# Kernel optimization log

Measured on AMD Instinct MI355X. Metric: run time of the kernel, lower is better.

## Reference

```python
import jax, jax.numpy as jnp
import numpy as np
from jax import lax

QBITS = 8  # per layer_configs: 8-bit weights and activations


def fake_quant(x, bits=QBITS):
    """Per-tensor symmetric fake quantization with straight-through estimator."""
    qmax = float(2 ** (bits - 1) - 1)  # 127 for 8-bit
    scale = jnp.maximum(jnp.max(jnp.abs(x)), 1e-8) / qmax
    q = jnp.clip(jnp.round(x / scale), -qmax - 1.0, qmax) * scale
    # STE: forward uses q, backward passes gradient through unchanged
    return x + lax.stop_gradient(q - x)


def qconv(x, w, b):
    """Fake-quantized conv: quantize activations and weights, then VALID conv + bias."""
    xq = fake_quant(x)
    wq = fake_quant(w)
    y = lax.conv_general_dilated(
        xq, wq, window_strides=(1, 1), padding='VALID',
        dimension_numbers=('NCHW', 'OIHW', 'NCHW'))
    return y + b[None, :, None, None]


def setup_inputs() -> dict:
    key = jax.random.key(0)
    ks = jax.random.split(key, 9)
    return {
        'x':  jax.random.uniform(ks[0], (256, 1, 128, 128), dtype=jnp.float32),
        'w1': jax.random.normal(ks[1], (16, 1, 3, 3), dtype=jnp.float32) * 0.3,
        'b1': jax.random.normal(ks[2], (16,), dtype=jnp.float32) * 0.05,
        'w2': jax.random.normal(ks[3], (16, 16, 3, 3), dtype=jnp.float32) * 0.1,
        'b2': jax.random.normal(ks[4], (16,), dtype=jnp.float32) * 0.05,
        'w3': jax.random.normal(ks[5], (16, 16, 3, 3), dtype=jnp.float32) * 0.1,
        'b3': jax.random.normal(ks[6], (16,), dtype=jnp.float32) * 0.05,
        'w4': jax.random.normal(ks[7], (1, 16, 2, 2), dtype=jnp.float32) * 0.1,
        'b4': jax.random.normal(ks[8], (1,), dtype=jnp.float32) * 0.05,
    }


def reference(x, w1, b1, w2, b2, w3, b3, w4, b4):
    # x: [N,1,128,128] -> [N,16,126,126] -> [N,16,124,124] -> [N,16,122,122] -> [N,1,121,121]
    h = jax.nn.relu(qconv(x, w1, b1))
    h = jax.nn.relu(qconv(h, w2, b2))
    h = jax.nn.relu(qconv(h, w3, b3))
    return jax.nn.sigmoid(qconv(h, w4, b4))
```

## Files before the change

### kernel.cpp

```cpp
#include <hip/hip_runtime.h>
#include <math.h>


#define THREADS 256

typedef __attribute__((ext_vector_type(4))) int i32x4;

__device__ __forceinline__ int xcd_swz(int bid, int nwg) {
    return (bid & 7) * (nwg >> 3) + (bid >> 3);
}

__device__ __forceinline__ float block_reduce_max(float m, float* wred) {
#pragma unroll
    for (int off = 32; off > 0; off >>= 1)
        m = fmaxf(m, __shfl_down(m, off, 64));
    if ((threadIdx.x & 63) == 0) wred[threadIdx.x >> 6] = m;
    __syncthreads();
    return fmaxf(fmaxf(wred[0], wred[1]), fmaxf(wred[2], wred[3]));
}

__global__ void init_kernel(unsigned int* slots) {
    if (threadIdx.x < 8) slots[threadIdx.x] = 0u;
}

__global__ void fill_kernel(float* out, int n, float v) {
    int i = blockIdx.x * blockDim.x + threadIdx.x;
    int stride = gridDim.x * blockDim.x;
    for (; i < n; i += stride) out[i] = v;
}

__global__ __launch_bounds__(THREADS) void absmax4_kernel(
    const float4* __restrict__ x, int n4, unsigned int* __restrict__ slot) {
    __shared__ float wred[4];
    float m = 0.f;
    const int stride = gridDim.x * blockDim.x;
    for (int i = blockIdx.x * blockDim.x + threadIdx.x; i < n4; i += stride) {
        float4 v = x[i];
        m = fmaxf(fmaxf(fabsf(v.x), fabsf(v.y)),
                  fmaxf(fmaxf(fabsf(v.z), fabsf(v.w)), m));
    }
    m = block_reduce_max(m, wred);
    if (threadIdx.x == 0) atomicMax(slot, __float_as_uint(m));
}

__global__ __launch_bounds__(THREADS) void quant_w_kernel(
    const float* __restrict__ w1, const float* __restrict__ w2,
    const float* __restrict__ w3, const float* __restrict__ w4,
    float* __restrict__ qw1, float* __restrict__ qw4,
    signed char* __restrict__ wi8_2, signed char* __restrict__ wi8_3,
    unsigned int* __restrict__ slots) {
    __shared__ float wred[4];
    const float* w; int nel;
    switch (blockIdx.x) {
        case 0:  w = w1; nel = 144;  break;
        case 1:  w = w2; nel = 2304; break;
        case 2:  w = w3; nel = 2304; break;
        default: w = w4; nel = 64;   break;
    }
    float m = 0.f;
    for (int i = threadIdx.x; i < nel; i += blockDim.x)
        m = fmaxf(m, fabsf(w[i]));
    m = block_reduce_max(m, wred);
    if (threadIdx.x == 0) slots[4 + blockIdx.x] = __float_as_uint(m);
    const float s = fmaxf(m, 1e-8f) / 127.0f;

    if (blockIdx.x == 0) {
        for (int i = threadIdx.x; i < 144; i += blockDim.x) {
            int p = i % 9, o = i / 9;
            float q = fminf(fmaxf(rintf(w[i] / s), -128.f), 127.f);
            qw1[p * 16 + o] = q * s;
        }
    } else if (blockIdx.x == 3) {
        for (int i = threadIdx.x; i < 64; i += blockDim.x) {
            float q = fminf(fmaxf(rintf(w[i] / s), -128.f), 127.f);
            qw4[i] = q * s;
        }
    } else {
        signed char* wi8 = (blockIdx.x == 1) ? wi8_2 : wi8_3;
        for (int i = threadIdx.x; i < 3072; i += blockDim.x) {
            int ci = i & 15, lane = (i >> 4) & 63, g = i >> 10;
            int co = lane & 15, qq = lane >> 4;
            int pos = 4 * g + qq;
            float v = 0.f;
            if (pos < 9) {
                int ky = pos / 3, kx = pos % 3;
                v = fminf(fmaxf(rintf(w[((co * 16 + ci) * 3 + ky) * 3 + kx] / s),
                                -128.f), 127.f);
            }
            wi8[i] = (signed char)(int)v;
        }
    }
}

template <int MODE>
__global__ __launch_bounds__(THREADS) void conv1_kernel(
    const float* __restrict__ x, const float* __restrict__ qw,
    const float* __restrict__ bias, signed char* __restrict__ out,
    unsigned int* __restrict__ slots) {
    constexpr int IH = 128, IW = 128, OH = 126, OW = 126;
    __shared__ float tile[34 * 34];
    __shared__ float wred[4];
    const int bid = xcd_swz(blockIdx.x, gridDim.x);
    const int n = bid >> 4, tr = bid & 15;
    const int oy0 = (tr >> 2) * 32, ox0 = (tr & 3) * 32;
    const float s_in = fmaxf(__uint_as_float(slots[0]), 1e-8f) / 127.0f;
    const float* xN = x + (size_t)n * IH * IW;

#pragma unroll
    for (int it = 0; it < 5; ++it) {
        int px = it * 256 + threadIdx.x;
        if (px < 1156) {
            int iy = px / 34, ix = px - iy * 34;
            int gy = min(oy0 + iy, IH - 1), gx = min(ox0 + ix, IW - 1);
            float q = rintf(xN[gy * IW + gx] / s_in);
            tile[px] = fminf(fmaxf(q, -128.f), 127.f);
        }
    }
    __syncthreads();

    const int tx = (threadIdx.x & 15) * 2, ty = (threadIdx.x >> 4) * 2;
    float m = 0.f;
    float s_out = 0.f;
    if constexpr (MODE == 2)
        s_out = fmaxf(__uint_as_float(slots[1]), 1e-8f) / 127.0f;

#pragma unroll
    for (int sy = 0; sy < 2; ++sy)
#pragma unroll
    for (int sx = 0; sx < 2; ++sx) {
        const int py = ty + sy, pxx = tx + sx;
        float acc[16];
#pragma unroll
        for (int c = 0; c < 16; ++c) acc[c] = 0.f;
#pragma unroll
        for (int p = 0; p < 9; ++p) {
            const float xv = tile[(py + p / 3) * 34 + pxx + p % 3];
            const float* wp = qw + p * 16;
#pragma unroll
            for (int co = 0; co < 16; ++co)
                acc[co] = fmaf(xv, wp[co], acc[co]);
        }
        const int oy = oy0 + py, ox = ox0 + pxx;
        const bool ok = (oy < OH) && (ox < OW);
        if constexpr (MODE == 1) {
#pragma unroll
            for (int co = 0; co < 16; ++co) {
                float y = fmaxf(fmaf(acc[co], s_in, bias[co]), 0.f);
                if (ok) m = fmaxf(m, y);
            }
        } else {
            unsigned pk[4] = {0u, 0u, 0u, 0u};
#pragma unroll
            for (int co = 0; co < 16; ++co) {
                float y = fmaxf(fmaf(acc[co], s_in, bias[co]), 0.f);
                float q8 = fminf(fmaxf(rintf(y / s_out), -128.f), 127.f);
                pk[co >> 2] |= ((unsigned)(int)q8 & 0xffu) << ((co & 3) * 8);
            }
            if (ok) {
                int4 v; v.x = pk[0]; v.y = pk[1]; v.z = pk[2]; v.w = pk[3];
                *(int4*)(out + ((size_t)(n * OH + oy) * OW + ox) * 16) = v;
            }
        }
    }
    if constexpr (MODE == 1) {
        m = block_reduce_max(m, wred);
        if (threadIdx.x == 0) atomicMax(&slots[1], __float_as_uint(m));
    }
}

template <bool STORE>
__global__ __launch_bounds__(THREADS) void mconv_kernel(
    const signed char* __restrict__ in, const signed char* __restrict__ wi8,
    const float* __restrict__ bias, signed char* __restrict__ out,
    unsigned int* __restrict__ slots, int in_slot, int w_slot, int out_slot,
    int IH, int IW) {
    __shared__ signed char tile[1156 * 16];
    __shared__ float wred[4];
    const int OH = IH - 2, OW = IW - 2;
    const int bid = xcd_swz(blockIdx.x, gridDim.x);
    const int n = bid >> 4, tr = bid & 15;
    const int oy0 = (tr >> 2) * 32, ox0 = (tr & 3) * 32;

    const int tid = threadIdx.x, lane = tid & 63, wv = tid >> 6;
    const int q = lane >> 4, col = lane & 15;

    const signed char* inN = in + (size_t)n * IH * IW * 16;

#pragma unroll
    for (int it = 0; it < 5; ++it) {
        int px = it * 256 + tid;
        if (px < 1156) {
            int iy = px / 34, ix = px - iy * 34;
            int gy = min(oy0 + iy, IH - 1), gx = min(ox0 + ix, IW - 1);
            *(int4*)(tile + px * 16) =
                *(const int4*)(inN + ((size_t)gy * IW + gx) * 16);
        }
    }

    i32x4 afrag[3];
#pragma unroll
    for (int g = 0; g < 3; ++g)
        afrag[g] = ((const i32x4*)wi8)[g * 64 + lane];

    __syncthreads();

    int poff[3];
#pragma unroll
    for (int g = 0; g < 3; ++g) {
        int pos = 4 * g + q;
        int dy = (pos < 9) ? pos / 3 : 0;
        int dx = (pos < 9) ? pos % 3 : 0;
        poff[g] = (dy * 34 + dx) * 16;
    }
    const int wr = wv >> 1, wc = wv & 1;
    const int bx = 16 * wc + col;
    const int ox = ox0 + bx;

    const float s_in = fmaxf(__uint_as_float(slots[in_slot]), 1e-8f) / 127.0f;
    const float s_w  = fmaxf(__uint_as_float(slots[w_slot]),  1e-8f) / 127.0f;
    const float sxw = s_in * s_w;
    float bj[4];
#pragma unroll
    for (int j = 0; j < 4; ++j) bj[j] = bias[q * 4 + j];
    float s_out = 0.f;
    if constexpr (STORE)
        s_out = fmaxf(__uint_as_float(slots[out_slot]), 1e-8f) / 127.0f;

    signed char* outN = out + (size_t)n * OH * OW * 16;
    float m = 0.f;

#pragma unroll 4
    for (int r = 0; r < 16; ++r) {
        const int iy = 16 * wr + r;
        const int base = (iy * 34 + bx) * 16;
        i32x4 acc = {0, 0, 0, 0};
#pragma unroll
        for (int g = 0; g < 3; ++g) {
            i32x4 b = *(const i32x4*)(tile + base + poff[g]);
            acc = __builtin_amdgcn_mfma_i32_16x16x64_i8(afrag[g], b, acc, 0, 0, 0);
        }
        const int oy = oy0 + iy;
        const bool ok = (oy < OH) && (ox < OW);
        if constexpr (STORE) {
            unsigned pk = 0u;
#pragma unroll
            for (int j = 0; j < 4; ++j) {
                float y = fmaxf(fmaf((float)acc[j], sxw, bj[j]), 0.f);
                float q8 = fminf(fmaxf(rintf(y / s_out), -128.f), 127.f);
                pk |= ((unsigned)(int)q8 & 0xffu) << (j * 8);
            }
            if (ok)
                *(unsigned*)(outN + ((size_t)oy * OW + ox) * 16 + q * 4) = pk;
        } else {
#pragma unroll
            for (int j = 0; j < 4; ++j) {
                float y = fmaxf(fmaf((float)acc[j], sxw, bj[j]), 0.f);
                if (ok) m = fmaxf(m, y);
            }
        }
    }
    if constexpr (!STORE) {
        m = block_reduce_max(m, wred);
        if (tid == 0) atomicMax(&slots[out_slot], __float_as_uint(m));
    }
}

__global__ __launch_bounds__(THREADS) void conv4_kernel(
    const signed char* __restrict__ in, const float* __restrict__ qw,
    const float* __restrict__ bias, float* __restrict__ out,
    unsigned int* __restrict__ slots) {
    constexpr int IH = 122, IW = 122, OH = 121, OW = 121;
    const int bid = xcd_swz(blockIdx.x, gridDim.x);
    const int n = bid >> 4, tr = bid & 15;
    const int oyb = (tr >> 2) * 32 + ((threadIdx.x >> 4) * 2);
    const int oxb = (tr & 3) * 32 + ((threadIdx.x & 15) * 2);
    const float s_in = fmaxf(__uint_as_float(slots[3]), 1e-8f) / 127.0f;
    const float b0 = bias[0];
    const signed char* inN = in + (size_t)n * IH * IW * 16;

    float w[64];
#pragma unroll
    for (int i = 0; i < 64; ++i) w[i] = qw[i];

#pragma unroll
    for (int sy = 0; sy < 2; ++sy)
#pragma unroll
    for (int sx = 0; sx < 2; ++sx) {
        const int oy = oyb + sy, ox = oxb + sx;
        if (oy >= OH || ox >= OW) continue;
        float acc = 0.f;
#pragma unroll
        for (int ky = 0; ky < 2; ++ky)
#pragma unroll
        for (int kx = 0; kx < 2; ++kx) {
            union { int4 v; signed char c[16]; } u;
            u.v = *(const int4*)(inN + ((size_t)(oy + ky) * IW + ox + kx) * 16);
#pragma unroll
            for (int ci = 0; ci < 16; ++ci)
                acc = fmaf((float)u.c[ci], w[(ci * 2 + ky) * 2 + kx], acc);
        }
        float y = fmaf(acc, s_in, b0);
        out[(size_t)(n * OH + oy) * OW + ox] = 1.0f / (1.0f + expf(-y));
    }
}

extern "C" void kernel_launch(void* const* d_in, const int* in_sizes, int n_in,
                              void* d_out, int out_size, void* d_ws, size_t ws_size,
                              hipStream_t stream) {
    (void)in_sizes; (void)n_in;
    const float* x  = (const float*)d_in[0];
    const float* w1 = (const float*)d_in[1];
    const float* b1 = (const float*)d_in[2];
    const float* w2 = (const float*)d_in[3];
    const float* b2 = (const float*)d_in[4];
    const float* w3 = (const float*)d_in[5];
    const float* b3 = (const float*)d_in[6];
    const float* w4 = (const float*)d_in[7];
    const float* b4 = (const float*)d_in[8];

    char* ws = (char*)d_ws;
    unsigned int* slots = (unsigned int*)ws;
    float* qw1 = (float*)(ws + 256);
    float* qw4 = (float*)(ws + 1024);
    signed char* wi8_2 = (signed char*)(ws + 2048);
    signed char* wi8_3 = (signed char*)(ws + 5120);

    const size_t Q1 = 65028096ULL;
    const size_t Q2 = 62980096ULL;
    signed char* qb1 = (signed char*)(ws + 32768);
    signed char* qb2 = (signed char*)(ws + 32768 + Q1);
    float* outp = (float*)d_out;

    const size_t need = 32768ULL + Q1 + Q2;
    if (ws_size < need) {
        float v = 100.0f + (float)(ws_size >> 20);
        hipLaunchKernelGGL(fill_kernel, dim3(1024), dim3(THREADS), 0, stream,
                           outp, out_size, v);
        return;
    }

    const int blocks = 256 * 16;

    hipLaunchKernelGGL(init_kernel, dim3(1), dim3(64), 0, stream, slots);
    hipLaunchKernelGGL(absmax4_kernel, dim3(2048), dim3(THREADS), 0, stream,
                       (const float4*)x, 256 * 128 * 128 / 4, slots + 0);
    hipLaunchKernelGGL(quant_w_kernel, dim3(4), dim3(THREADS), 0, stream,
                       w1, w2, w3, w4, qw1, qw4, wi8_2, wi8_3, slots);

    hipLaunchKernelGGL((conv1_kernel<1>), dim3(blocks), dim3(THREADS), 0, stream,
                       x, qw1, b1, nullptr, slots);
    hipLaunchKernelGGL((conv1_kernel<2>), dim3(blocks), dim3(THREADS), 0, stream,
                       x, qw1, b1, qb1, slots);
    hipLaunchKernelGGL((mconv_kernel<false>), dim3(blocks), dim3(THREADS), 0, stream,
                       qb1, wi8_2, b2, nullptr, slots, 1, 5, 2, 126, 126);
    hipLaunchKernelGGL((mconv_kernel<true>), dim3(blocks), dim3(THREADS), 0, stream,
                       qb1, wi8_2, b2, qb2, slots, 1, 5, 2, 126, 126);
    hipLaunchKernelGGL((mconv_kernel<false>), dim3(blocks), dim3(THREADS), 0, stream,
                       qb2, wi8_3, b3, nullptr, slots, 2, 6, 3, 124, 124);
    hipLaunchKernelGGL((mconv_kernel<true>), dim3(blocks), dim3(THREADS), 0, stream,
                       qb2, wi8_3, b3, qb1, slots, 2, 6, 3, 124, 124);
    hipLaunchKernelGGL(conv4_kernel, dim3(blocks), dim3(THREADS), 0, stream,
                       qb1, qw4, b4, outp, slots);
}
```

Baseline: 384.7 us.

## Swizzle int8 LDS tile, hoist conv1 patch to registers, defer epilogue for max pass

The int8 MFMA conv kernel now stores its LDS tile with an XOR swizzle on 16-byte records, meant to cut bank conflicts on the strided fragment reads; the buffer gets 128 bytes of padding to hold the swizzled range. Conv1 loads its 4x4 input patch into registers once instead of re-reading shared memory for every tap. The max-only passes keep a raw per-channel accumulator maximum and apply scale, bias and ReLU once at the end rather than per pixel. The requant path multiplies by a reciprocal scale instead of dividing and drops the redundant lower clamp. The reciprocal can differ from true division in rare rounding-boundary cases, which could flip an int8 code.

```diff
diff --git a/kernel.cpp b/kernel.cpp
--- a/kernel.cpp
+++ b/kernel.cpp
@@ -8,6 +8,10 @@
 
 __device__ __forceinline__ int xcd_swz(int bid, int nwg) {
     return (bid & 7) * (nwg >> 3) + (bid >> 3);
+}
+
+__device__ __forceinline__ int swzb(int rec) {
+    return (rec << 4) ^ ((rec & 56) << 1);
 }
 
 __device__ __forceinline__ float block_reduce_max(float m, float* wred) {
@@ -119,42 +123,54 @@
     __syncthreads();
 
     const int tx = (threadIdx.x & 15) * 2, ty = (threadIdx.x >> 4) * 2;
-    float m = 0.f;
-    float s_out = 0.f;
+
+    float p[4][4];
+#pragma unroll
+    for (int r = 0; r < 4; ++r) {
+        const float* rp = &tile[(ty + r) * 34 + tx];
+        p[r][0] = rp[0]; p[r][1] = rp[1]; p[r][2] = rp[2]; p[r][3] = rp[3];
+    }
+
+    float r_out = 0.f;
     if constexpr (MODE == 2)
-        s_out = fmaxf(__uint_as_float(slots[1]), 1e-8f) / 127.0f;
+        r_out = 127.0f / fmaxf(__uint_as_float(slots[1]), 1e-8f);
+
+    float accm[16];
+#pragma unroll
+    for (int c = 0; c < 16; ++c) accm[c] = -3.0e38f;
 
 #pragma unroll
     for (int sy = 0; sy < 2; ++sy)
 #pragma unroll
     for (int sx = 0; sx < 2; ++sx) {
-        const int py = ty + sy, pxx = tx + sx;
         float acc[16];
 #pragma unroll
         for (int c = 0; c < 16; ++c) acc[c] = 0.f;
 #pragma unroll
-        for (int p = 0; p < 9; ++p) {
-            const float xv = tile[(py + p / 3) * 34 + pxx + p % 3];
-            const float* wp = qw + p * 16;
+        for (int ky = 0; ky < 3; ++ky)
+#pragma unroll
+        for (int kx = 0; kx < 3; ++kx) {
+            const float xv = p[sy + ky][sx + kx];
+            const float* wp = qw + (ky * 3 + kx) * 16;
 #pragma unroll
             for (int co = 0; co < 16; ++co)
                 acc[co] = fmaf(xv, wp[co], acc[co]);
         }
-        const int oy = oy0 + py, ox = ox0 + pxx;
+        const int oy = oy0 + ty + sy, ox = ox0 + tx + sx;
         const bool ok = (oy < OH) && (ox < OW);
         if constexpr (MODE == 1) {
+            if (ok) {
+#pragma unroll
+                for (int co = 0; co < 16; ++co)
+                    accm[co] = fmaxf(accm[co], acc[co]);
+            }
+        } else {
+            unsigned pk[4] = {0u, 0u, 0u, 0u};
 #pragma unroll
             for (int co = 0; co < 16; ++co) {
                 float y = fmaxf(fmaf(acc[co], s_in, bias[co]), 0.f);
-                if (ok) m = fmaxf(m, y);
-            }
-        } else {
-            unsigned pk[4] = {0u, 0u, 0u, 0u};
-#pragma unroll
-            for (int co = 0; co < 16; ++co) {
-                float y = fmaxf(fmaf(acc[co], s_in, bias[co]), 0.f);
-                float q8 = fminf(fmaxf(rintf(y / s_out), -128.f), 127.f);
-                pk[co >> 2] |= ((unsigned)(int)q8 & 0xffu) << ((co & 3) * 8);
+                float q8 = fminf(rintf(y * r_out), 127.f);
+                pk[co >> 2] |= ((unsigned)(int)q8) << ((co & 3) * 8);
             }
             if (ok) {
                 int4 v; v.x = pk[0]; v.y = pk[1]; v.z = pk[2]; v.w = pk[3];
@@ -163,6 +179,10 @@
         }
     }
     if constexpr (MODE == 1) {
+        float m = 0.f;
+#pragma unroll
+        for (int co = 0; co < 16; ++co)
+            m = fmaxf(m, fmaxf(fmaf(accm[co], s_in, bias[co]), 0.f));
         m = block_reduce_max(m, wred);
         if (threadIdx.x == 0) atomicMax(&slots[1], __float_as_uint(m));
     }
@@ -174,7 +194,7 @@
     const float* __restrict__ bias, signed char* __restrict__ out,
     unsigned int* __restrict__ slots, int in_slot, int w_slot, int out_slot,
     int IH, int IW) {
-    __shared__ signed char tile[1156 * 16];
+    __shared__ signed char tile[1156 * 16 + 128];
     __shared__ float wred[4];
     const int OH = IH - 2, OW = IW - 2;
     const int bid = xcd_swz(blockIdx.x, gridDim.x);
@@ -192,7 +212,7 @@
         if (px < 1156) {
             int iy = px / 34, ix = px - iy * 34;
             int gy = min(oy0 + iy, IH - 1), gx = min(ox0 + ix, IW - 1);
-            *(int4*)(tile + px * 16) =
+            *(int4*)(tile + swzb(px)) =
                 *(const int4*)(inN + ((size_t)gy * IW + gx) * 16);
         }
     }
@@ -204,13 +224,13 @@
 
     __syncthreads();
 
-    int poff[3];
+    int drec[3];
 #pragma unroll
     for (int g = 0; g < 3; ++g) {
         int pos = 4 * g + q;
         int dy = (pos < 9) ? pos / 3 : 0;
         int dx = (pos < 9) ? pos % 3 : 0;
-        poff[g] = (dy * 34 + dx) * 16;
+        drec[g] = dy * 34 + dx;
     }
     const int wr = wv >> 1, wc = wv & 1;
     const int bx = 16 * wc + col;
@@ -222,21 +242,23 @@
     float bj[4];
 #pragma unroll
     for (int j = 0; j < 4; ++j) bj[j] = bias[q * 4 + j];
-    float s_out = 0.f;
+    float r_out = 0.f;
     if constexpr (STORE)
-        s_out = fmaxf(__uint_as_float(slots[out_slot]), 1e-8f) / 127.0f;
+        r_out = 127.0f / fmaxf(__uint_as_float(slots[out_slot]), 1e-8f);
 
     signed char* outN = out + (size_t)n * OH * OW * 16;
-    float m = 0.f;
+    int mi[4];
+#pragma unroll
+    for (int j = 0; j < 4; ++j) mi[j] = INT_MIN;
 
 #pragma unroll 4
     for (int r = 0; r < 16; ++r) {
         const int iy = 16 * wr + r;
-        const int base = (iy * 34 + bx) * 16;
+        const int rec = iy * 34 + bx;
         i32x4 acc = {0, 0, 0, 0};
 #pragma unroll
         for (int g = 0; g < 3; ++g) {
-            i32x4 b = *(const i32x4*)(tile + base + poff[g]);
+            i32x4 b = *(const i32x4*)(tile + swzb(rec + drec[g]));
             acc = __builtin_amdgcn_mfma_i32_16x16x64_i8(afrag[g], b, acc, 0, 0, 0);
         }
         const int oy = oy0 + iy;
@@ -246,20 +268,24 @@
 #pragma unroll
             for (int j = 0; j < 4; ++j) {
                 float y = fmaxf(fmaf((float)acc[j], sxw, bj[j]), 0.f);
-                float q8 = fminf(fmaxf(rintf(y / s_out), -128.f), 127.f);
-                pk |= ((unsigned)(int)q8 & 0xffu) << (j * 8);
+                float q8 = fminf(rintf(y * r_out), 127.f);
+                pk |= ((unsigned)(int)q8) << (j * 8);
             }
             if (ok)
                 *(unsigned*)(outN + ((size_t)oy * OW + ox) * 16 + q * 4) = pk;
         } else {
-#pragma unroll
-            for (int j = 0; j < 4; ++j) {
-                float y = fmaxf(fmaf((float)acc[j], sxw, bj[j]), 0.f);
-                if (ok) m = fmaxf(m, y);
+            if (ok) {
+#pragma unroll
+                for (int j = 0; j < 4; ++j)
+                    mi[j] = (acc[j] > mi[j]) ? acc[j] : mi[j];
             }
         }
     }
     if constexpr (!STORE) {
+        float m = 0.f;
+#pragma unroll
+        for (int j = 0; j < 4; ++j)
+            m = fmaxf(m, fmaxf(fmaf((float)mi[j], sxw, bj[j]), 0.f));
         m = block_reduce_max(m, wred);
         if (tid == 0) atomicMax(&slots[out_slot], __float_as_uint(m));
     }
```

New measurement: 333.5 us. 13.3% less time.
